# Kernel tuning notes

Hardware: AMD Instinct MI355X
Metric: run time of the kernel (lower is better)

## Reference

```python
import jax, jax.numpy as jnp
import numpy as np


def setup_inputs() -> dict:
    key = jax.random.key(0)
    ks = jax.random.split(key, 8)
    B, T, U, O = 2048, 2048, 16, 8
    w = lambda k, shape: (jax.random.normal(k, shape, dtype=jnp.float32) * 0.1)
    return {
        "num_inputs": 16,
        "enc_output": jax.random.normal(ks[0], (B, T, U), dtype=jnp.float32),
        "hidden": jax.random.normal(ks[1], (B, U), dtype=jnp.float32),
        "w1": w(ks[2], (U, U)),                 # Dense(16, use_bias=False)
        "w2_k": w(ks[3], (U, U)), "w2_b": jnp.zeros((U,), jnp.float32),
        "w3_k": w(ks[4], (U, 1)), "w3_b": jnp.zeros((1,), jnp.float32),
        "gru_k": w(ks[5], (U, 3 * U)),          # input kernel  [z|r|h]
        "gru_rk": w(ks[6], (U, 3 * U)),         # recurrent kernel [z|r|h]
        "gru_b": jnp.zeros((3 * U,), jnp.float32),
        "dense_k": w(ks[7], (U, O)), "dense_b": jnp.zeros((O,), jnp.float32),
    }


def _gru_step(x, h, k, rk, b):
    """Keras GRU cell (reset_after=False), gate order z, r, h."""
    xz, xr, xh = jnp.split(x @ k + b, 3, axis=-1)
    hz, hr, hh_ = jnp.split(h @ rk, 3, axis=-1)
    z = jax.nn.sigmoid(xz + hz)
    r = jax.nn.sigmoid(xr + hr)
    hh = jnp.tanh(xh + r * hh_)
    return z * h + (1.0 - z) * hh


def reference(num_inputs, enc_output, hidden, w1, w2_k, w2_b, w3_k, w3_b,
              gru_k, gru_rk, gru_b, dense_k, dense_b):
    # Loop-invariant part of the Bahdanau score: w1(enc_output)  [B,T,U]
    enc_w1 = jnp.einsum('btu,uv->btv', enc_output, w1)
    # Original code calls self.gru(x) with NO initial state -> h0 = zeros each step.
    h0 = jnp.zeros_like(hidden)

    def step(h_attn, _):
        q = h_attn @ w2_k + w2_b                                # [B,U]
        score = jnp.tanh(enc_w1 + q[:, None, :]) @ w3_k + w3_b  # [B,T,1]
        attn = jax.nn.softmax(score, axis=1)                    # over T
        ctx = jnp.sum(attn * enc_output, axis=1)                # [B,U]
        new_h = _gru_step(ctx, h0, gru_k, gru_rk, gru_b)        # GRU state
        out = new_h @ dense_k + dense_b                         # [B,O]
        return new_h, out

    _, outs = jax.lax.scan(step, hidden, None, length=num_inputs)  # [S,B,O]
    return jnp.transpose(outs, (1, 0, 2))  # [B, num_inputs, O]
```

## Files before the change

### kernel.cpp

```cpp
#include <hip/hip_runtime.h>
#include <stdint.h>

#define NTHREADS 512
#define C2F 2.8853900817779268f
#define C1F 1.4426950408889634f

__device__ __forceinline__ float asflt(uint32_t u) {
    union { uint32_t u; float f; } x; x.u = u; return x.f;
}
__device__ __forceinline__ uint32_t bf16rne(float f) {
    uint32_t u = __float_as_uint(f);
    return (u + 0x7FFFu + ((u >> 16) & 1u)) >> 16;
}

__global__ __launch_bounds__(NTHREADS)
__attribute__((amdgpu_waves_per_eu(4, 4)))
void decoder_kernel(const int* __restrict__ nin,
                    const float* __restrict__ enc,
                    const float* __restrict__ hidden,
                    const float* __restrict__ w1,
                    const float* __restrict__ w2k,
                    const float* __restrict__ w2b,
                    const float* __restrict__ w3k,
                    const float* __restrict__ gruk,
                    const float* __restrict__ grub,
                    const float* __restrict__ dek,
                    const float* __restrict__ deb,
                    float* __restrict__ out)
{
    extern __shared__ char smem[];
    float* F    = (float*)(smem + 65536);
    float* wred = F;
    float* lred = F + 128;
    float* Qbuf = F + 136;
    float* hbuf = F + 152;
    float* ctxb = F + 168;
    float* w2bl = F + 184;
    float* gbzl = F + 200;
    float* gbhl = F + 216;
    float* dbl  = F + 232;
    float* w2l  = F + 240;
    float* gkzl = F + 496;
    float* gkhl = F + 752;
    float* dkl  = F + 1008;

    const int tid  = threadIdx.x;
    const int b    = blockIdx.x;
    const int S    = nin[0];
    const int lane = tid & 63;
    const int wv   = tid >> 6;

    if (tid < 256) {
        w2l[tid] = w2k[tid];
        int m = tid >> 4, v = tid & 15;
        gkzl[tid] = gruk[m * 48 + v];
        gkhl[tid] = gruk[m * 48 + 32 + v];
    }
    if (tid < 128) dkl[tid] = dek[tid];
    if (tid < 16) {
        w2bl[tid] = w2b[tid];
        gbzl[tid] = grub[tid];
        gbhl[tid] = grub[32 + tid];
    }
    if (tid < 8) dbl[tid] = deb[tid];

    {
        const float4* eg = (const float4*)enc + (size_t)b * 8192;
        #pragma unroll
        for (int i = 0; i < 16; ++i) {
            int f = tid + NTHREADS * i;
            float4 vv = eg[f];
            int t = f >> 2, q = f & 3;
            uint2 w;
            w.x = bf16rne(vv.x) | (bf16rne(vv.y) << 16);
            w.y = bf16rne(vv.z) | (bf16rne(vv.w) << 16);
            *(uint2*)(smem + q * 16384 + t * 8) = w;
        }
    }
    __syncthreads();

    uint32_t Epack[32];
    #pragma unroll
    for (int k = 0; k < 4; ++k) {
        const int t = tid + 512 * k;
        float acc[16];
        #pragma unroll
        for (int v = 0; v < 16; ++v) acc[v] = 0.0f;
        #pragma unroll
        for (int q = 0; q < 4; ++q) {
            uint2 w = *(const uint2*)(smem + q * 16384 + t * 8);
            float e0 = asflt(w.x << 16), e1 = asflt(w.x & 0xFFFF0000u);
            float e2 = asflt(w.y << 16), e3 = asflt(w.y & 0xFFFF0000u);
            #pragma unroll
            for (int v = 0; v < 16; ++v) {
                acc[v] = fmaf(e0, w1[(4 * q + 0) * 16 + v], acc[v]);
                acc[v] = fmaf(e1, w1[(4 * q + 1) * 16 + v], acc[v]);
                acc[v] = fmaf(e2, w1[(4 * q + 2) * 16 + v], acc[v]);
                acc[v] = fmaf(e3, w1[(4 * q + 3) * 16 + v], acc[v]);
            }
        }
        #pragma unroll
        for (int v = 0; v < 16; ++v) {
            uint32_t h = bf16rne(__builtin_amdgcn_exp2f(C2F * acc[v]));
            if ((k & 1) == 0) Epack[v * 2 + (k >> 1)] = h;
            else              Epack[v * 2 + (k >> 1)] |= h << 16;
        }
    }
    float n3r[16];
    #pragma unroll
    for (int u = 0; u < 16; ++u) n3r[u] = -2.0f * w3k[u];

    if (wv == 0) {
        if (lane < 16) hbuf[lane] = hidden[b * 16 + lane];
        int u = lane & 15;
        float q = w2bl[u];
        #pragma unroll
        for (int m = 0; m < 16; ++m) q = fmaf(hbuf[m], w2l[m * 16 + u], q);
        if (lane < 16) Qbuf[u] = __builtin_amdgcn_exp2f(C2F * q);
    }
    __syncthreads();

    for (int s = 0; s < S; ++s) {
        float Qr[16];
        #pragma unroll
        for (int u = 0; u < 16; ++u) Qr[u] = Qbuf[u];
        float a0 = 0.f, a1 = 0.f, a2 = 0.f, a3 = 0.f;
        #pragma unroll
        for (int u = 0; u < 16; ++u) {
            uint32_t pA = Epack[u * 2 + 0], pB = Epack[u * 2 + 1];
            float E0 = asflt(pA << 16), E1 = asflt(pA & 0xFFFF0000u);
            float E2 = asflt(pB << 16), E3 = asflt(pB & 0xFFFF0000u);
            float qu = Qr[u], nu = n3r[u];
            a0 = fmaf(nu, __builtin_amdgcn_rcpf(fmaf(E0, qu, 1.0f)), a0);
            a1 = fmaf(nu, __builtin_amdgcn_rcpf(fmaf(E1, qu, 1.0f)), a1);
            a2 = fmaf(nu, __builtin_amdgcn_rcpf(fmaf(E2, qu, 1.0f)), a2);
            a3 = fmaf(nu, __builtin_amdgcn_rcpf(fmaf(E3, qu, 1.0f)), a3);
        }
        float p0 = __builtin_amdgcn_exp2f(C1F * a0);
        float p1 = __builtin_amdgcn_exp2f(C1F * a1);
        float p2 = __builtin_amdgcn_exp2f(C1F * a2);
        float p3 = __builtin_amdgcn_exp2f(C1F * a3);

        float cx[16];
        #pragma unroll
        for (int q = 0; q < 4; ++q) {
            const char* pb = smem + q * 16384;
            uint2 w0 = *(const uint2*)(pb + (tid       ) * 8);
            uint2 w1_ = *(const uint2*)(pb + (tid + 512) * 8);
            uint2 w2_ = *(const uint2*)(pb + (tid + 1024) * 8);
            uint2 w3_ = *(const uint2*)(pb + (tid + 1536) * 8);
            float c0, c1, c2, c3;
            c0 = p0 * asflt(w0.x << 16);          c1 = p0 * asflt(w0.x & 0xFFFF0000u);
            c2 = p0 * asflt(w0.y << 16);          c3 = p0 * asflt(w0.y & 0xFFFF0000u);
            c0 = fmaf(p1, asflt(w1_.x << 16), c0); c1 = fmaf(p1, asflt(w1_.x & 0xFFFF0000u), c1);
            c2 = fmaf(p1, asflt(w1_.y << 16), c2); c3 = fmaf(p1, asflt(w1_.y & 0xFFFF0000u), c3);
            c0 = fmaf(p2, asflt(w2_.x << 16), c0); c1 = fmaf(p2, asflt(w2_.x & 0xFFFF0000u), c1);
            c2 = fmaf(p2, asflt(w2_.y << 16), c2); c3 = fmaf(p2, asflt(w2_.y & 0xFFFF0000u), c3);
            c0 = fmaf(p3, asflt(w3_.x << 16), c0); c1 = fmaf(p3, asflt(w3_.x & 0xFFFF0000u), c1);
            c2 = fmaf(p3, asflt(w3_.y << 16), c2); c3 = fmaf(p3, asflt(w3_.y & 0xFFFF0000u), c3);
            cx[q * 4 + 0] = c0; cx[q * 4 + 1] = c1; cx[q * 4 + 2] = c2; cx[q * 4 + 3] = c3;
        }
        #pragma unroll
        for (int st = 0; st < 4; ++st) {
            const int half = 8 >> st;
            const int bit = (lane >> st) & 1;
            #pragma unroll
            for (int j = 0; j < half; ++j) {
                float lo = cx[j], hi = cx[half + j];
                float mine  = bit ? hi : lo;
                float other = bit ? lo : hi;
                other = __shfl_xor(other, 1 << st, 64);
                cx[j] = mine + other;
            }
        }
        cx[0] += __shfl_xor(cx[0], 16, 64);
        cx[0] += __shfl_xor(cx[0], 32, 64);
        if (lane < 16) {
            int c = ((lane & 1) << 3) | ((lane & 2) << 1) | ((lane & 4) >> 1) | ((lane & 8) >> 3);
            wred[wv * 16 + c] = cx[0];
        }
        float lp = (p0 + p1) + (p2 + p3);
        #pragma unroll
        for (int m = 1; m < 64; m <<= 1) lp += __shfl_xor(lp, m, 64);
        if (lane == 0) lred[wv] = lp;
        __syncthreads();

        if (wv == 0) {
            int v = lane & 15;
            float l = 0.f;
            #pragma unroll
            for (int m = 0; m < 8; ++m) l += lred[m];
            float ctx = 0.f;
            #pragma unroll
            for (int m = 0; m < 8; ++m) ctx += wred[m * 16 + v];
            ctx *= __builtin_amdgcn_rcpf(l);
            if (lane < 16) ctxb[v] = ctx;
            float xz = gbzl[v], xh = gbhl[v];
            #pragma unroll
            for (int m = 0; m < 16; ++m) {
                float cm = ctxb[m];
                xz = fmaf(cm, gkzl[m * 16 + v], xz);
                xh = fmaf(cm, gkhl[m * 16 + v], xh);
            }
            float z  = __builtin_amdgcn_rcpf(1.0f + __builtin_amdgcn_exp2f(-C1F * xz));
            float eh = __builtin_amdgcn_exp2f(C2F * xh);
            float hh = fmaf(-2.0f, __builtin_amdgcn_rcpf(eh + 1.0f), 1.0f);
            float hn = (1.0f - z) * hh;
            if (lane < 16) hbuf[v] = hn;
            int o = lane & 7;
            float ov = dbl[o];
            #pragma unroll
            for (int u = 0; u < 16; ++u) ov = fmaf(hbuf[u], dkl[u * 8 + o], ov);
            if (lane < 8) out[(size_t)b * (S * 8) + s * 8 + o] = ov;
            float q = w2bl[v];
            #pragma unroll
            for (int m = 0; m < 16; ++m) q = fmaf(hbuf[m], w2l[m * 16 + v], q);
            if (lane < 16) Qbuf[v] = __builtin_amdgcn_exp2f(C2F * q);
        }
        __syncthreads();
    }
}

#define SMEM_BYTES 70144

extern "C" void kernel_launch(void* const* d_in, const int* in_sizes, int n_in,
                              void* d_out, int out_size, void* d_ws, size_t ws_size,
                              hipStream_t stream) {
    (void)in_sizes; (void)n_in; (void)d_ws; (void)ws_size; (void)out_size;
    const int*   nin    = (const int*)d_in[0];
    const float* enc    = (const float*)d_in[1];
    const float* hidden = (const float*)d_in[2];
    const float* w1     = (const float*)d_in[3];
    const float* w2k    = (const float*)d_in[4];
    const float* w2b    = (const float*)d_in[5];
    const float* w3k    = (const float*)d_in[6];
    const float* gruk   = (const float*)d_in[8];
    const float* grub   = (const float*)d_in[10];
    const float* dek    = (const float*)d_in[11];
    const float* deb    = (const float*)d_in[12];
    float* outp = (float*)d_out;

    hipFuncSetAttribute(reinterpret_cast<const void*>(&decoder_kernel),
                        hipFuncAttributeMaxDynamicSharedMemorySize, SMEM_BYTES);
    decoder_kernel<<<2048, NTHREADS, SMEM_BYTES, stream>>>(
        nin, enc, hidden, w1, w2k, w2b, w3k, gruk, grub, dek, deb, outp);
}
```

Before: 689.4 us.

## Double block size to 1024 threads with two timesteps per thread

The block grows from 512 to 1024 threads, so each thread now handles 2 timesteps instead of 4. This halves the per-thread register footprint for the packed exp values and shortens the serial per-step work. The waves_per_eu attribute is dropped and the reduction buffers grow to cover 16 waves. Q values are loaded per step through readfirstlane as scalars, and w3 is reloaded inside the loop. The trade-off is more waves per block and a longer final reduction. Shared memory use still allows about two blocks per CU, so occupancy may not rise and barrier cost may grow.

```diff
diff --git a/kernel.cpp b/kernel.cpp
--- a/kernel.cpp
+++ b/kernel.cpp
@@ -1,7 +1,7 @@
 #include <hip/hip_runtime.h>
 #include <stdint.h>
 
-#define NTHREADS 512
+#define NTHREADS 1024
 #define C2F 2.8853900817779268f
 #define C1F 1.4426950408889634f
 
@@ -14,7 +14,6 @@
 }
 
 __global__ __launch_bounds__(NTHREADS)
-__attribute__((amdgpu_waves_per_eu(4, 4)))
 void decoder_kernel(const int* __restrict__ nin,
                     const float* __restrict__ enc,
                     const float* __restrict__ hidden,
@@ -31,18 +30,18 @@
     extern __shared__ char smem[];
     float* F    = (float*)(smem + 65536);
     float* wred = F;
-    float* lred = F + 128;
-    float* Qbuf = F + 136;
-    float* hbuf = F + 152;
-    float* ctxb = F + 168;
-    float* w2bl = F + 184;
-    float* gbzl = F + 200;
-    float* gbhl = F + 216;
-    float* dbl  = F + 232;
-    float* w2l  = F + 240;
-    float* gkzl = F + 496;
-    float* gkhl = F + 752;
-    float* dkl  = F + 1008;
+    float* lred = F + 256;
+    float* Qbuf = F + 272;
+    float* hbuf = F + 288;
+    float* ctxb = F + 304;
+    float* w2bl = F + 320;
+    float* gbzl = F + 336;
+    float* gbhl = F + 352;
+    float* dbl  = F + 368;
+    float* w2l  = F + 376;
+    float* gkzl = F + 632;
+    float* gkhl = F + 888;
+    float* dkl  = F + 1144;
 
     const int tid  = threadIdx.x;
     const int b    = blockIdx.x;
@@ -67,7 +66,7 @@
     {
         const float4* eg = (const float4*)enc + (size_t)b * 8192;
         #pragma unroll
-        for (int i = 0; i < 16; ++i) {
+        for (int i = 0; i < 8; ++i) {
             int f = tid + NTHREADS * i;
             float4 vv = eg[f];
             int t = f >> 2, q = f & 3;
@@ -79,10 +78,10 @@
     }
     __syncthreads();
 
-    uint32_t Epack[32];
+    uint32_t Epack[16];
     #pragma unroll
-    for (int k = 0; k < 4; ++k) {
-        const int t = tid + 512 * k;
+    for (int k = 0; k < 2; ++k) {
+        const int t = tid + NTHREADS * k;
         float acc[16];
         #pragma unroll
         for (int v = 0; v < 16; ++v) acc[v] = 0.0f;
@@ -102,13 +101,10 @@
         #pragma unroll
         for (int v = 0; v < 16; ++v) {
             uint32_t h = bf16rne(__builtin_amdgcn_exp2f(C2F * acc[v]));
-            if ((k & 1) == 0) Epack[v * 2 + (k >> 1)] = h;
-            else              Epack[v * 2 + (k >> 1)] |= h << 16;
-        }
-    }
-    float n3r[16];
-    #pragma unroll
-    for (int u = 0; u < 16; ++u) n3r[u] = -2.0f * w3k[u];
+            if (k == 0) Epack[v] = h;
+            else        Epack[v] |= h << 16;
+        }
+    }
 
     if (wv == 0) {
         if (lane < 16) hbuf[lane] = hidden[b * 16 + lane];
@@ -121,43 +117,31 @@
     __syncthreads();
 
     for (int s = 0; s < S; ++s) {
-        float Qr[16];
-        #pragma unroll
-        for (int u = 0; u < 16; ++u) Qr[u] = Qbuf[u];
-        float a0 = 0.f, a1 = 0.f, a2 = 0.f, a3 = 0.f;
+        float a0 = 0.f, a1 = 0.f;
         #pragma unroll
         for (int u = 0; u < 16; ++u) {
-            uint32_t pA = Epack[u * 2 + 0], pB = Epack[u * 2 + 1];
-            float E0 = asflt(pA << 16), E1 = asflt(pA & 0xFFFF0000u);
-            float E2 = asflt(pB << 16), E3 = asflt(pB & 0xFFFF0000u);
-            float qu = Qr[u], nu = n3r[u];
+            float qu = asflt((uint32_t)__builtin_amdgcn_readfirstlane(
+                                 (int)__float_as_uint(Qbuf[u])));
+            float nu = -2.0f * w3k[u];
+            uint32_t pk = Epack[u];
+            float E0 = asflt(pk << 16), E1 = asflt(pk & 0xFFFF0000u);
             a0 = fmaf(nu, __builtin_amdgcn_rcpf(fmaf(E0, qu, 1.0f)), a0);
             a1 = fmaf(nu, __builtin_amdgcn_rcpf(fmaf(E1, qu, 1.0f)), a1);
-            a2 = fmaf(nu, __builtin_amdgcn_rcpf(fmaf(E2, qu, 1.0f)), a2);
-            a3 = fmaf(nu, __builtin_amdgcn_rcpf(fmaf(E3, qu, 1.0f)), a3);
         }
         float p0 = __builtin_amdgcn_exp2f(C1F * a0);
         float p1 = __builtin_amdgcn_exp2f(C1F * a1);
-        float p2 = __builtin_amdgcn_exp2f(C1F * a2);
-        float p3 = __builtin_amdgcn_exp2f(C1F * a3);
 
         float cx[16];
         #pragma unroll
         for (int q = 0; q < 4; ++q) {
             const char* pb = smem + q * 16384;
-            uint2 w0 = *(const uint2*)(pb + (tid       ) * 8);
-            uint2 w1_ = *(const uint2*)(pb + (tid + 512) * 8);
-            uint2 w2_ = *(const uint2*)(pb + (tid + 1024) * 8);
-            uint2 w3_ = *(const uint2*)(pb + (tid + 1536) * 8);
+            uint2 w0  = *(const uint2*)(pb + (tid           ) * 8);
+            uint2 w1_ = *(const uint2*)(pb + (tid + NTHREADS) * 8);
             float c0, c1, c2, c3;
-            c0 = p0 * asflt(w0.x << 16);          c1 = p0 * asflt(w0.x & 0xFFFF0000u);
-            c2 = p0 * asflt(w0.y << 16);          c3 = p0 * asflt(w0.y & 0xFFFF0000u);
+            c0 = p0 * asflt(w0.x << 16);           c1 = p0 * asflt(w0.x & 0xFFFF0000u);
+            c2 = p0 * asflt(w0.y << 16);           c3 = p0 * asflt(w0.y & 0xFFFF0000u);
             c0 = fmaf(p1, asflt(w1_.x << 16), c0); c1 = fmaf(p1, asflt(w1_.x & 0xFFFF0000u), c1);
             c2 = fmaf(p1, asflt(w1_.y << 16), c2); c3 = fmaf(p1, asflt(w1_.y & 0xFFFF0000u), c3);
-            c0 = fmaf(p2, asflt(w2_.x << 16), c0); c1 = fmaf(p2, asflt(w2_.x & 0xFFFF0000u), c1);
-            c2 = fmaf(p2, asflt(w2_.y << 16), c2); c3 = fmaf(p2, asflt(w2_.y & 0xFFFF0000u), c3);
-            c0 = fmaf(p3, asflt(w3_.x << 16), c0); c1 = fmaf(p3, asflt(w3_.x & 0xFFFF0000u), c1);
-            c2 = fmaf(p3, asflt(w3_.y << 16), c2); c3 = fmaf(p3, asflt(w3_.y & 0xFFFF0000u), c3);
             cx[q * 4 + 0] = c0; cx[q * 4 + 1] = c1; cx[q * 4 + 2] = c2; cx[q * 4 + 3] = c3;
         }
         #pragma unroll
@@ -179,7 +163,7 @@
             int c = ((lane & 1) << 3) | ((lane & 2) << 1) | ((lane & 4) >> 1) | ((lane & 8) >> 3);
             wred[wv * 16 + c] = cx[0];
         }
-        float lp = (p0 + p1) + (p2 + p3);
+        float lp = p0 + p1;
         #pragma unroll
         for (int m = 1; m < 64; m <<= 1) lp += __shfl_xor(lp, m, 64);
         if (lane == 0) lred[wv] = lp;
@@ -189,10 +173,10 @@
             int v = lane & 15;
             float l = 0.f;
             #pragma unroll
-            for (int m = 0; m < 8; ++m) l += lred[m];
+            for (int m = 0; m < 16; ++m) l += lred[m];
             float ctx = 0.f;
             #pragma unroll
-            for (int m = 0; m < 8; ++m) ctx += wred[m * 16 + v];
+            for (int m = 0; m < 16; ++m) ctx += wred[m * 16 + v];
             ctx *= __builtin_amdgcn_rcpf(l);
             if (lane < 16) ctxb[v] = ctx;
             float xz = gbzl[v], xh = gbhl[v];
@@ -221,7 +205,7 @@
     }
 }
 
-#define SMEM_BYTES 70144
+#define SMEM_BYTES 70656
 
 extern "C" void kernel_launch(void* const* d_in, const int* in_sizes, int n_in,
                               void* d_out, int out_size, void* d_ws, size_t ws_size,
```

After: 840.5 us. 1.22x slower.
